# Kernel optimization log

Hardware: AMD Instinct MI355X
Metric: run time of the kernel (lower is better)

## Reference

```python
import jax, jax.numpy as jnp
import numpy as np

B, T, C, H = 8, 2048, 1024, 64

def setup_inputs() -> dict:
    key = jax.random.key(0)
    kx, kq, kk, kv = jax.random.split(key, 4)
    scale = 1.0 / np.sqrt(C)
    return {
        "x": jax.random.normal(kx, (B, T, C), dtype=jnp.float32),
        "Wq": jax.random.normal(kq, (C, H), dtype=jnp.float32) * scale,
        "Wk": jax.random.normal(kk, (C, H), dtype=jnp.float32) * scale,
        "Wv": jax.random.normal(kv, (C, H), dtype=jnp.float32) * scale,
    }

def reference(x, Wq, Wk, Wv):
    # q,k,v: [B,T,H]
    q = jnp.einsum('btc,ch->bth', x, Wq)
    k = jnp.einsum('btc,ch->bth', x, Wk)
    v = jnp.einsum('btc,ch->bth', x, Wv)
    scale = k.shape[-1] ** -0.5
    wei = jnp.einsum('bth,bsh->bts', q, k) * scale  # [B,T,T]
    causal = jnp.tril(jnp.ones((x.shape[1], x.shape[1]), dtype=bool))
    wei = jnp.where(causal, wei, -jnp.inf)
    wei = jax.nn.softmax(wei, axis=-1)
    out = jnp.einsum('bts,bsh->bth', wei, v)  # [B,T,H]
    return out
```

## Files before the change

kernel.cpp:

```cpp
#include <hip/hip_runtime.h>

#define B_ 8
#define T_ 2048
#define C_ 1024
#define H_ 64

typedef __bf16 bf16x8 __attribute__((ext_vector_type(8)));
typedef float  f32x4  __attribute__((ext_vector_type(4)));
typedef unsigned short u16x8 __attribute__((ext_vector_type(8)));

__device__ __forceinline__ unsigned short f2bf(float f) {
    unsigned u = __builtin_bit_cast(unsigned, f);
    u += 0x8000u;
    return (unsigned short)(u >> 16);
}

__device__ __forceinline__ float bf2f(unsigned short v) {
    unsigned u = ((unsigned)v) << 16;
    return __builtin_bit_cast(float, u);
}

__device__ __forceinline__ unsigned pack2(float lo, float hi) {
    unsigned a = __builtin_bit_cast(unsigned, lo) + 0x8000u;
    unsigned b = __builtin_bit_cast(unsigned, hi) + 0x8000u;
    return (a >> 16) | (b & 0xffff0000u);
}

union U8 { unsigned u32[4]; u16x8 v; };

__device__ __forceinline__ u16x8 cvt8(float4 f0, float4 f1) {
    U8 r;
    r.u32[0] = pack2(f0.x, f0.y);
    r.u32[1] = pack2(f0.z, f0.w);
    r.u32[2] = pack2(f1.x, f1.y);
    r.u32[3] = pack2(f1.z, f1.w);
    return r.v;
}

__device__ __forceinline__ bf16x8 load8_bf(const unsigned short* p) {
    return __builtin_bit_cast(bf16x8, *(const u16x8*)p);
}


__global__ void cast_weights(const float* __restrict__ Wq,
                             const float* __restrict__ Wk,
                             const float* __restrict__ Wv,
                             unsigned short* __restrict__ Wtf) {
    int idx = blockIdx.x * blockDim.x + threadIdx.x;
    int n   = idx % 192;
    int c   = idx / 192;
    int w   = n >> 6;
    int h   = n & 63;
    const float* W = (w == 0) ? Wq : (w == 1) ? Wk : Wv;
    int nt = n >> 4, l16 = n & 15;
    int kk = c >> 5, quad = (c >> 3) & 3, j = c & 7;
    Wtf[(size_t)(nt * 32 + kk) * 512 + l16 * 32 + quad * 8 + j] =
        f2bf(W[(size_t)c * H_ + h]);
}

__global__ __launch_bounds__(256, 4) void qkv_proj(
        const float* __restrict__ x,
        const unsigned short* __restrict__ Wtf,
        unsigned short* __restrict__ Qf,
        unsigned short* __restrict__ Kf,
        unsigned short* __restrict__ Vf) {
    __shared__ __attribute__((aligned(16))) unsigned short As_[16 * 1024];

    const int tid  = threadIdx.x;
    const int ns   = tid >> 6;
    const int lane = tid & 63;
    const int l16  = lane & 15;
    const int quad = lane >> 4;
    const size_t r0 = (size_t)blockIdx.x * 16;
    const int bb     = (int)(r0 >> 11);
    const int tloc0  = (int)(r0 & (T_ - 1));
    const int t16_0  = tloc0 >> 4;
    const int s32    = tloc0 >> 5;
    const int half16 = t16_0 & 1;

    f32x4 acc[3];
#pragma unroll
    for (int i = 0; i < 3; i++) acc[i] = (f32x4){0.f, 0.f, 0.f, 0.f};

    const int sw   = l16 & 7;
    const int loff = l16 * 32 + quad * 8;

#pragma unroll
    for (int i = 0; i < 8; i++) {
        int c   = i * 256 + tid;
        int row = c >> 7;
        int g   = c & 127;
        const float* sp = x + (r0 + row) * C_ + g * 8;
        float4 f0 = *(const float4*)sp;
        float4 f1 = *(const float4*)(sp + 4);
        int off = row * 1024 + ((g & ~7) + ((g & 7) ^ (row & 7))) * 8;
        *(u16x8*)(&As_[off]) = cvt8(f0, f1);
    }
    __syncthreads();

#pragma unroll 4
    for (int kk = 0; kk < 32; kk++) {
        int g  = kk * 4 + quad;
        int gs = ((g & ~7) + ((g & 7) ^ sw)) * 8;
        bf16x8 a0 = load8_bf(&As_[l16 * 1024 + gs]);
#pragma unroll
        for (int i = 0; i < 3; i++) {
            bf16x8 b = load8_bf(Wtf + (size_t)((ns * 3 + i) * 32 + kk) * 512 + loff);
            acc[i] = __builtin_amdgcn_mfma_f32_16x16x32_bf16(a0, b, acc[i], 0, 0, 0);
        }
    }

    __syncthreads();
    unsigned short* E = As_;
#pragma unroll
    for (int i = 0; i < 3; i++) {
        int nt = ns * 3 + i;
#pragma unroll
        for (int r = 0; r < 4; r++) {
            unsigned short bv = f2bf(acc[i][r]);
            int off;
            if (nt < 4) {
                off = (nt >> 1) * 512 + (quad * 4 + r) * 32 +
                      ((nt & 1) * 2 + (l16 >> 3)) * 8 + (l16 & 7);
            } else if (nt < 8) {
                int nk = nt - 4;
                off = 1024 + (nk >> 1) * 512 + (quad * 4 + r) * 32 +
                      ((nk & 1) * 2 + (l16 >> 3)) * 8 + (l16 & 7);
            } else {
                int ht = nt - 8;
                off = 2048 + ht * 256 + l16 * 16 + quad * 4 + r;
            }
            E[off] = bv;
        }
    }
    __syncthreads();

    {
        int ch = tid >> 6;
        int g  = tid & 63;
        unsigned short* dst = (ch < 2) ? Qf : Kf;
        int part = ch & 1;
        dst += ((size_t)(bb * 128 + t16_0) * 2 + part) * 512;
        *(u16x8*)(dst + g * 8) = *(const u16x8*)(&E[ch * 512 + g * 8]);
    }
    if (tid < 128) {
        int ht   = tid >> 5;
        int rr   = tid & 31;
        int l16v = rr >> 1;
        int hh   = rr & 1;
        unsigned short* dst = Vf + ((size_t)(bb * 64 + s32) * 4 + ht) * 512
                              + l16v * 32 + half16 * 16 + hh * 8;
        *(u16x8*)dst = *(const u16x8*)(&E[2048 + ht * 256 + l16v * 16 + hh * 8]);
    }
}

#define PROW 33
#define OMS2 66

__global__ __launch_bounds__(256) void attn(
        const unsigned short* __restrict__ Qf,
        const unsigned short* __restrict__ Kf,
        const unsigned short* __restrict__ Vf,
        float* __restrict__ out) {
    __shared__ unsigned int ps_[4 * 32 * PROW];
    __shared__ unsigned short Om_[4 * 32 * OMS2];
    __shared__ float mred_[4][32];
    __shared__ float lred_[4][32];

    const int tid  = threadIdx.x;
    const int wave = tid >> 6;
    const int lane = tid & 63;
    const int l16  = lane & 15;
    const int quad = lane >> 4;
    const int b    = blockIdx.x & 7;
    const int qt32 = blockIdx.x >> 3;
    const int q0   = qt32 * 32;
    const int tdiag = qt32 >> 1;

    const int loff = l16 * 32 + quad * 8;

    bf16x8 qf[2][2];
#pragma unroll
    for (int qg = 0; qg < 2; qg++) {
        const unsigned short* Qfb = Qf + (size_t)((b * 128 + qt32 * 2 + qg) * 2) * 512;
        qf[qg][0] = load8_bf(Qfb + loff);
        qf[qg][1] = load8_bf(Qfb + 512 + loff);
    }

    f32x4 o[8];
#pragma unroll
    for (int i = 0; i < 8; i++) o[i] = (f32x4){0.f, 0.f, 0.f, 0.f};
    float m_run[2] = {-1e30f, -1e30f}, l_run[2] = {0.f, 0.f};

    const float scale = 0.125f;
    const unsigned short* Kfb = Kf + (size_t)b * 128 * 1024;
    const unsigned short* Vfb = Vf + (size_t)b * 64 * 2048;
    unsigned int* Pw = &ps_[wave * 32 * PROW];

    for (int t = wave; t <= tdiag; t += 4) {
        bf16x8 vf[8];
#pragma unroll
        for (int ks = 0; ks < 2; ks++)
#pragma unroll
            for (int ht = 0; ht < 4; ht++)
                vf[ht * 2 + ks] = load8_bf(
                    Vfb + ((size_t)(t * 2 + ks) * 4 + ht) * 512 + loff);

        f32x4 s[2][4];
#pragma unroll
        for (int nt = 0; nt < 4; nt++) {
            const unsigned short* kp = Kfb + (size_t)(t * 4 + nt) * 1024;
            bf16x8 kf0 = load8_bf(kp + loff);
            bf16x8 kf1 = load8_bf(kp + 512 + loff);
#pragma unroll
            for (int qg = 0; qg < 2; qg++) {
                f32x4 z = (f32x4){0.f, 0.f, 0.f, 0.f};
                z = __builtin_amdgcn_mfma_f32_16x16x32_bf16(kf0, qf[qg][0], z, 0, 0, 0);
                z = __builtin_amdgcn_mfma_f32_16x16x32_bf16(kf1, qf[qg][1], z, 0, 0, 0);
                s[qg][nt] = z;
            }
        }

#pragma unroll
        for (int qg = 0; qg < 2; qg++)
#pragma unroll
            for (int nt = 0; nt < 4; nt++)
#pragma unroll
                for (int r = 0; r < 4; r++) s[qg][nt][r] *= scale;

        if (t == tdiag) {
#pragma unroll
            for (int qg = 0; qg < 2; qg++) {
                int q = q0 + qg * 16 + l16;
#pragma unroll
                for (int nt = 0; nt < 4; nt++)
#pragma unroll
                    for (int r = 0; r < 4; r++) {
                        int key = t * 64 + nt * 16 + quad * 4 + r;
                        if (key > q) s[qg][nt][r] = -1e30f;
                    }
            }
        }

#pragma unroll
        for (int qg = 0; qg < 2; qg++) {
            float m0 = fmaxf(fmaxf(s[qg][0][0], s[qg][0][1]), fmaxf(s[qg][0][2], s[qg][0][3]));
            float m1 = fmaxf(fmaxf(s[qg][1][0], s[qg][1][1]), fmaxf(s[qg][1][2], s[qg][1][3]));
            float m2 = fmaxf(fmaxf(s[qg][2][0], s[qg][2][1]), fmaxf(s[qg][2][2], s[qg][2][3]));
            float m3 = fmaxf(fmaxf(s[qg][3][0], s[qg][3][1]), fmaxf(s[qg][3][2], s[qg][3][3]));
            float mx = fmaxf(fmaxf(m0, m1), fmaxf(m2, m3));
            mx = fmaxf(mx, __shfl_xor(mx, 16));
            mx = fmaxf(mx, __shfl_xor(mx, 32));
            const float m_new = fmaxf(m_run[qg], mx);
            const float alpha = __expf(m_run[qg] - m_new);
            m_run[qg] = m_new;

            float rs = 0.f;
#pragma unroll
            for (int nt = 0; nt < 4; nt++) {
#pragma unroll
                for (int i = 0; i < 2; i++) {
                    float p0 = __expf(s[qg][nt][2 * i]     - m_new);
                    float p1 = __expf(s[qg][nt][2 * i + 1] - m_new);
                    rs += p0 + p1;
                    Pw[(qg * 16 + l16) * PROW + nt * 8 + quad * 2 + i] = pack2(p0, p1);
                }
            }
            rs += __shfl_xor(rs, 16);
            rs += __shfl_xor(rs, 32);
            l_run[qg] = l_run[qg] * alpha + rs;

#pragma unroll
            for (int ht = 0; ht < 4; ht++)
#pragma unroll
                for (int r = 0; r < 4; r++) o[qg * 4 + ht][r] *= alpha;
        }

#pragma unroll
        for (int ks = 0; ks < 2; ks++) {
#pragma unroll
            for (int qg = 0; qg < 2; qg++) {
                bf16x8 pB = __builtin_bit_cast(bf16x8,
                    *(const u16x8*)(&Pw[(qg * 16 + l16) * PROW + ks * 16 + quad * 4]));
#pragma unroll
                for (int ht = 0; ht < 4; ht++)
                    o[qg * 4 + ht] = __builtin_amdgcn_mfma_f32_16x16x32_bf16(
                        vf[ht * 2 + ks], pB, o[qg * 4 + ht], 0, 0, 0);
            }
        }
    }

#pragma unroll
    for (int qg = 0; qg < 2; qg++) {
#pragma unroll
        for (int ht = 0; ht < 4; ht++)
#pragma unroll
            for (int r = 0; r < 4; r++)
                Om_[(wave * 32 + qg * 16 + l16) * OMS2 + ht * 16 + quad * 4 + r] =
                    f2bf(o[qg * 4 + ht][r]);
        if (quad == 0) {
            mred_[wave][qg * 16 + l16] = m_run[qg];
            lred_[wave][qg * 16 + l16] = l_run[qg];
        }
    }
    __syncthreads();

    const int hcol = tid & 63;
    const int qr0  = tid >> 6;
#pragma unroll
    for (int qq = 0; qq < 8; qq++) {
        const int q = qr0 + qq * 4;
        float M = -1e30f;
#pragma unroll
        for (int w = 0; w < 4; w++) M = fmaxf(M, mred_[w][q]);
        float lt = 0.f, ov = 0.f;
#pragma unroll
        for (int w = 0; w < 4; w++) {
            float e = __expf(mred_[w][q] - M);
            lt += e * lred_[w][q];
            ov += e * bf2f(Om_[(w * 32 + q) * OMS2 + hcol]);
        }
        out[((size_t)b * T_ + q0 + q) * H_ + hcol] = ov / lt;
    }
}

extern "C" void kernel_launch(void* const* d_in, const int* in_sizes, int n_in,
                              void* d_out, int out_size, void* d_ws, size_t ws_size,
                              hipStream_t stream) {
    const float* x  = (const float*)d_in[0];
    const float* Wq = (const float*)d_in[1];
    const float* Wk = (const float*)d_in[2];
    const float* Wv = (const float*)d_in[3];
    float* out = (float*)d_out;

    unsigned short* Qf  = (unsigned short*)d_ws;
    unsigned short* Kf  = Qf + (size_t)B_ * T_ * H_;
    unsigned short* Vf  = Kf + (size_t)B_ * T_ * H_;
    unsigned short* Wtf = Vf + (size_t)B_ * T_ * H_;

    cast_weights<<<(192 * C_) / 256, 256, 0, stream>>>(Wq, Wk, Wv, Wtf);
    qkv_proj<<<B_ * T_ / 16, 256, 0, stream>>>(x, Wtf, Qf, Kf, Vf);
    attn<<<B_ * (T_ / 32), 256, 0, stream>>>(Qf, Kf, Vf, out);
}
```

Baseline: 139.6 us.

## Stage x tile into LDS as fp32 via global_load_lds, convert at MFMA time

The QKV projection now copies the fp32 x tile straight into shared memory with direct global-to-LDS loads (XOR-swizzled), so the bulk copy no longer goes through registers. The fp32-to-bf16 conversion moves into the MFMA loop, where each wave converts its own fragment. This doubles LDS use to 64KB per block and lowers launch bounds occupancy from 4 to 2 blocks. The cost is repeated conversion work: all four waves convert the same A fragments.

After: 138.1 us. Within noise of the previous version (-1.1%).

```diff
diff --git a/kernel.cpp b/kernel.cpp
--- a/kernel.cpp
+++ b/kernel.cpp
@@ -39,6 +39,12 @@
 
 __device__ __forceinline__ bf16x8 load8_bf(const unsigned short* p) {
     return __builtin_bit_cast(bf16x8, *(const u16x8*)p);
+}
+
+__device__ __forceinline__ void gload_lds16(const float* g, float* l) {
+    __builtin_amdgcn_global_load_lds(
+        (const __attribute__((address_space(1))) unsigned int*)g,
+        (__attribute__((address_space(3))) unsigned int*)l, 16, 0, 0);
 }
 
 
@@ -58,13 +64,13 @@
         f2bf(W[(size_t)c * H_ + h]);
 }
 
-__global__ __launch_bounds__(256, 4) void qkv_proj(
+__global__ __launch_bounds__(256, 2) void qkv_proj(
         const float* __restrict__ x,
         const unsigned short* __restrict__ Wtf,
         unsigned short* __restrict__ Qf,
         unsigned short* __restrict__ Kf,
         unsigned short* __restrict__ Vf) {
-    __shared__ __attribute__((aligned(16))) unsigned short As_[16 * 1024];
+    __shared__ __attribute__((aligned(16))) float Axs[16 * 1024];
 
     const int tid  = threadIdx.x;
     const int ns   = tid >> 6;
@@ -78,40 +84,43 @@
     const int s32    = tloc0 >> 5;
     const int half16 = t16_0 & 1;
 
+#pragma unroll
+    for (int jj = 0; jj < 16; jj++) {
+        int j   = ns * 16 + jj;
+        int row = j >> 2;
+        int S0  = (j & 3) * 64;
+        int g   = (S0 + lane) ^ (row & 7);
+        const float* gp = x + (r0 + row) * C_ + g * 4;
+        float* lp = &Axs[row * 1024 + S0 * 4];
+        gload_lds16(gp, lp);
+    }
+
     f32x4 acc[3];
 #pragma unroll
     for (int i = 0; i < 3; i++) acc[i] = (f32x4){0.f, 0.f, 0.f, 0.f};
 
-    const int sw   = l16 & 7;
-    const int loff = l16 * 32 + quad * 8;
-
-#pragma unroll
-    for (int i = 0; i < 8; i++) {
-        int c   = i * 256 + tid;
-        int row = c >> 7;
-        int g   = c & 127;
-        const float* sp = x + (r0 + row) * C_ + g * 8;
-        float4 f0 = *(const float4*)sp;
-        float4 f1 = *(const float4*)(sp + 4);
-        int off = row * 1024 + ((g & ~7) + ((g & 7) ^ (row & 7))) * 8;
-        *(u16x8*)(&As_[off]) = cvt8(f0, f1);
-    }
+    const int xsw = l16 & 7;
+    const unsigned short* wp = Wtf + (size_t)(ns * 3 * 32) * 512
+                               + l16 * 32 + quad * 8;
+    const float* Arow = &Axs[l16 * 1024];
+
     __syncthreads();
 
 #pragma unroll 4
     for (int kk = 0; kk < 32; kk++) {
-        int g  = kk * 4 + quad;
-        int gs = ((g & ~7) + ((g & 7) ^ sw)) * 8;
-        bf16x8 a0 = load8_bf(&As_[l16 * 1024 + gs]);
+        int g0 = kk * 8 + quad * 2;
+        float4 f0 = *(const float4*)(Arow + (size_t)((g0    ) ^ xsw) * 4);
+        float4 f1 = *(const float4*)(Arow + (size_t)((g0 + 1) ^ xsw) * 4);
+        bf16x8 a0 = __builtin_bit_cast(bf16x8, cvt8(f0, f1));
 #pragma unroll
         for (int i = 0; i < 3; i++) {
-            bf16x8 b = load8_bf(Wtf + (size_t)((ns * 3 + i) * 32 + kk) * 512 + loff);
+            bf16x8 b = load8_bf(wp + (size_t)(i * 32 + kk) * 512);
             acc[i] = __builtin_amdgcn_mfma_f32_16x16x32_bf16(a0, b, acc[i], 0, 0, 0);
         }
     }
 
     __syncthreads();
-    unsigned short* E = As_;
+    unsigned short* E = (unsigned short*)Axs;
 #pragma unroll
     for (int i = 0; i < 3; i++) {
         int nt = ns * 3 + i;
```
